# Performance work log

Hardware: AMD Instinct MI355X
Metric: run time of the kernel (lower is better)

The kernel has to match this reference:

```python
import jax, jax.numpy as jnp
import numpy as np

B, S, D = 4, 2048, 1024

def setup_inputs() -> dict:
    key = jax.random.key(0)
    k1, k2, k3, k4 = jax.random.split(key, 4)
    output = jax.random.normal(k1, (B, S, D), dtype=jnp.float32)
    # nn.Linear(dim, dim, bias=False): y = x @ W.T ; store W as [D, D]
    scale = 1.0 / np.sqrt(D)
    w_q = jax.random.uniform(k2, (D, D), dtype=jnp.float32, minval=-scale, maxval=scale)
    w_k = jax.random.uniform(k3, (D, D), dtype=jnp.float32, minval=-scale, maxval=scale)
    w_v = jax.random.uniform(k4, (D, D), dtype=jnp.float32, minval=-scale, maxval=scale)
    return {"output": output, "w_q": w_q, "w_k": w_k, "w_v": w_v}

def reference(output, w_q, w_k, w_v):
    # projections: x @ W.T (torch Linear convention)
    q = jnp.einsum('bsd,ed->bse', output, w_q)
    k = jnp.einsum('bsd,ed->bse', output, w_k)
    v = jnp.einsum('bsd,ed->bse', output, w_v)
    scores = jnp.einsum('bqd,bkd->bqk', q, k)      # unscaled, no mask
    attn = jax.nn.softmax(scores, axis=-1)
    return jnp.einsum('bqk,bkd->bqd', attn, v)
```

## Files before the change

### kernel.cpp

```cpp
#include <hip/hip_runtime.h>
#include <hip/hip_bf16.h>
#include <stdint.h>


typedef __attribute__((ext_vector_type(8))) _Float16 f16x8;
typedef __attribute__((ext_vector_type(4))) float f32x4;
typedef __attribute__((ext_vector_type(4))) unsigned short u16x4;

__device__ inline unsigned short f2h(float f) {
    union { _Float16 h; unsigned short u; } x;
    x.h = (_Float16)f;
    return x.u;
}
__device__ inline float h2f(unsigned short u) {
    union { unsigned short u; _Float16 h; } x;
    x.u = u;
    return (float)x.h;
}

__device__ inline void async16(const unsigned short* g, unsigned short* l) {
    __builtin_amdgcn_global_load_lds(
        (__attribute__((address_space(1))) void*)g,
        (__attribute__((address_space(3))) void*)l, 16, 0, 0);
}

template <int MODE, int BN>
__global__ __launch_bounds__(512)
void gemm512(const unsigned short* __restrict__ A,
             const unsigned short* __restrict__ B,
             void* __restrict__ C, void* __restrict__ C2,
             int K, int ldA, int ldB, int ldC,
             long sAz, long sBz, long sCz)
{
    constexpr int NT = BN / 32;
    constexpr int BI = BN / 64;
    __shared__ __align__(16) unsigned short smem[256 * 64 + BN * 64];
    unsigned short* As = smem;
    unsigned short* Bs = smem + 256 * 64;

    const int tid  = threadIdx.x;
    const int lane = tid & 63;
    const int wave = tid >> 6;
    const int wr   = wave >> 1, wc = wave & 1;
    const int quad = lane >> 4, lrow = lane & 15;
    const int bm   = blockIdx.x, bn = blockIdx.y, z = blockIdx.z;

    const unsigned short* Az = A + (long)z * sAz;
    const unsigned short* Bz = B + (long)z * sBz;

    const unsigned short* gA[4];
    const unsigned short* gB[BI];
#pragma unroll
    for (int i = 0; i < 4; ++i) {
        const int l = tid + 512 * i;
        const int r = l >> 3;
        const int c = (l & 7) ^ (r & 7);
        gA[i] = Az + (long)(bm * 256 + r) * ldA + c * 8;
    }
#pragma unroll
    for (int i = 0; i < BI; ++i) {
        const int l = tid + 512 * i;
        const int r = l >> 3;
        const int c = (l & 7) ^ (r & 7);
        gB[i] = Bz + (long)(bn * BN + r) * ldB + c * 8;
    }

    f32x4 acc[4][NT];
#pragma unroll
    for (int i = 0; i < 4; ++i)
#pragma unroll
        for (int j = 0; j < NT; ++j)
            acc[i][j] = f32x4{0.f, 0.f, 0.f, 0.f};

    const int fr = lrow & 7;

    for (int k0 = 0; k0 < K; k0 += 64) {
#pragma unroll
        for (int i = 0; i < 4; ++i) async16(gA[i], &As[(tid + 512 * i) * 8]);
#pragma unroll
        for (int i = 0; i < BI; ++i) async16(gB[i], &Bs[(tid + 512 * i) * 8]);
#pragma unroll
        for (int i = 0; i < 4; ++i) gA[i] += 64;
#pragma unroll
        for (int i = 0; i < BI; ++i) gB[i] += 64;
        __syncthreads();

#pragma unroll
        for (int ks = 0; ks < 2; ++ks) {
            const int pc = (((ks << 2) + quad) ^ fr) * 8;
            f16x8 af[4], bf[NT];
#pragma unroll
            for (int mt = 0; mt < 4; ++mt)
                af[mt] = *(const f16x8*)&As[(wr * 64 + mt * 16 + lrow) * 64 + pc];
#pragma unroll
            for (int nt = 0; nt < NT; ++nt)
                bf[nt] = *(const f16x8*)&Bs[(wc * (BN / 2) + nt * 16 + lrow) * 64 + pc];
#pragma unroll
            for (int mt = 0; mt < 4; ++mt)
#pragma unroll
                for (int nt = 0; nt < NT; ++nt)
                    acc[mt][nt] = __builtin_amdgcn_mfma_f32_16x16x32_f16(
                        af[mt], bf[nt], acc[mt][nt], 0, 0, 0);
        }
        __syncthreads();
    }

    const int col_base = bn * BN + wc * (BN / 2);

    if (MODE != 0 || z < 2) {
        const int row_base = bm * 256 + wr * 64;
        const long zC = (long)z * sCz;
#pragma unroll
        for (int mt = 0; mt < 4; ++mt)
#pragma unroll
            for (int nt = 0; nt < NT; ++nt)
#pragma unroll
                for (int r = 0; r < 4; ++r) {
                    const int row = row_base + mt * 16 + quad * 4 + r;
                    const int col = col_base + nt * 16 + lrow;
                    if (MODE == 2)
                        ((float*)C)[zC + (long)row * ldC + col] = acc[mt][nt][r];
                    else
                        ((unsigned short*)C)[zC + (long)row * ldC + col] =
                            f2h(acc[mt][nt][r]);
                }
    } else {
        unsigned short* T = smem;
#pragma unroll
        for (int p = 0; p < 4; ++p) {
            __syncthreads();
            if (wr == p) {
#pragma unroll
                for (int mt = 0; mt < 4; ++mt)
#pragma unroll
                    for (int nt = 0; nt < NT; ++nt) {
                        const int row_l = mt * 16 + quad * 4;
                        const int col_l = wc * 64 + nt * 16 + lrow;
                        u16x4 pk = {f2h(acc[mt][nt][0]), f2h(acc[mt][nt][1]),
                                    f2h(acc[mt][nt][2]), f2h(acc[mt][nt][3])};
                        *(u16x4*)&T[col_l * 72 + row_l] = pk;
                    }
            }
            __syncthreads();
            const int c  = tid >> 2;
            const int j0 = (tid & 3) * 16;
            const int tok0 = bm * 256 + p * 64;
            const int bb = tok0 >> 11;
            const int s0 = (tok0 & 2047) + j0;
            unsigned short* dst = (unsigned short*)C2 + (long)bb * 2097152 +
                                  (long)(bn * 128 + c) * 2048 + s0;
            const unsigned short* srcT = &T[c * 72 + j0];
            *(f16x8*)dst = *(const f16x8*)srcT;
            *(f16x8*)(dst + 8) = *(const f16x8*)(srcT + 8);
        }
    }
}

__global__ __launch_bounds__(256)
void cvt_all(const float* __restrict__ x, const float* __restrict__ w0,
             const float* __restrict__ w1, const float* __restrict__ w2,
             unsigned short* __restrict__ xh, unsigned short* __restrict__ wh)
{
    const int bid = blockIdx.x;
    const float* s;
    unsigned short* d;
    long i;
    if (bid < 4096) {
        s = x; d = xh;
        i = ((long)bid * 256 + threadIdx.x) * 8;
    } else {
        const int wid = bid - 4096;
        const int w = wid >> 9;
        s = (w == 0) ? w0 : (w == 1) ? w1 : w2;
        d = wh + (long)w * 1048576;
        i = ((long)(wid & 511) * 256 + threadIdx.x) * 8;
    }
    f32x4 a = *(const f32x4*)(s + i);
    f32x4 b = *(const f32x4*)(s + i + 4);
    union { unsigned short u[8]; f16x8 v; } t;
#pragma unroll
    for (int j = 0; j < 4; ++j) { t.u[j] = f2h(a[j]); t.u[4 + j] = f2h(b[j]); }
    *(f16x8*)(d + i) = t.v;
}

__global__ __launch_bounds__(256)
void softmax16(unsigned short* __restrict__ sc)
{
    const long row = blockIdx.x;
    unsigned short* srow = sc + row * 2048;
    const int tid = threadIdx.x;

    union { u16x4 p[2]; unsigned short u[8]; } in;
    in.p[0] = *(const u16x4*)(srow + tid * 8);
    in.p[1] = *(const u16x4*)(srow + tid * 8 + 4);
    float v[8];
#pragma unroll
    for (int i = 0; i < 8; ++i) v[i] = h2f(in.u[i]);

    float m = v[0];
#pragma unroll
    for (int i = 1; i < 8; ++i) m = fmaxf(m, v[i]);
#pragma unroll
    for (int off = 32; off; off >>= 1) m = fmaxf(m, __shfl_xor(m, off));

    __shared__ float redm[4], reds[4];
    if ((tid & 63) == 0) redm[tid >> 6] = m;
    __syncthreads();
    m = fmaxf(fmaxf(redm[0], redm[1]), fmaxf(redm[2], redm[3]));

    float s = 0.f;
#pragma unroll
    for (int i = 0; i < 8; ++i) { v[i] = __expf(v[i] - m); s += v[i]; }
#pragma unroll
    for (int off = 32; off; off >>= 1) s += __shfl_xor(s, off);
    if ((tid & 63) == 0) reds[tid >> 6] = s;
    __syncthreads();
    s = reds[0] + reds[1] + reds[2] + reds[3];

    const float inv = 1.f / s;
    union { unsigned short u[8]; f16x8 w; } t;
#pragma unroll
    for (int i = 0; i < 8; ++i) t.u[i] = f2h(v[i] * inv);
    *(f16x8*)(srow + tid * 8) = t.w;
}

extern "C" void kernel_launch(void* const* d_in, const int* in_sizes, int n_in,
                              void* d_out, int out_size, void* d_ws, size_t ws_size,
                              hipStream_t stream)
{
    const float* x  = (const float*)d_in[0];
    const float* wq = (const float*)d_in[1];
    const float* wk = (const float*)d_in[2];
    const float* wv = (const float*)d_in[3];
    float* out = (float*)d_out;

    char* base = (char*)d_ws;
    const bool batched = (ws_size >= 88080384UL);

    unsigned short* xh = (unsigned short*)base;
    unsigned short* wh = (unsigned short*)(base + 16777216);
    unsigned short* sc = (unsigned short*)base;
    unsigned short* q  = (unsigned short*)(base + (batched ? 33554432 : 23068672));
    unsigned short* k  = q + 8388608;
    unsigned short* vt = k + 8388608;

    cvt_all<<<5632, 256, 0, stream>>>(x, wq, wk, wv, xh, wh);

    gemm512<0, 128><<<dim3(32, 8, 3), 512, 0, stream>>>(
        xh, wh, q, vt, 1024, 1024, 1024, 1024, 0L, 1048576L, 8388608L);

    if (batched) {
        gemm512<1, 128><<<dim3(8, 16, 4), 512, 0, stream>>>(
            q, k, sc, nullptr, 1024, 1024, 1024, 2048,
            2097152L, 2097152L, 4194304L);
        softmax16<<<8192, 256, 0, stream>>>(sc);
        gemm512<2, 64><<<dim3(8, 16, 4), 512, 0, stream>>>(
            sc, vt, out, nullptr, 2048, 2048, 2048, 1024,
            4194304L, 2097152L, 2097152L);
    } else {
        for (int b = 0; b < 4; ++b) {
            gemm512<1, 128><<<dim3(8, 16, 1), 512, 0, stream>>>(
                q + (long)b * 2097152, k + (long)b * 2097152, sc, nullptr,
                1024, 1024, 1024, 2048, 0L, 0L, 0L);
            softmax16<<<2048, 256, 0, stream>>>(sc);
            gemm512<2, 64><<<dim3(8, 16, 1), 512, 0, stream>>>(
                sc, vt + (long)b * 2097152, out + (long)b * 2097152, nullptr,
                2048, 2048, 2048, 1024, 0L, 0L, 0L);
        }
    }
}
```

Before: 243.9 us.

## Switch GEMMs to 128x128 tiles with 2 waves using 32x32x16 MFMA

Replaces the 512-thread, 256-row-tile GEMM with a 128-thread kernel that computes 128x128 tiles, each wave owning a 128x64 slab. It uses the 32x32x16 f16 MFMA, which has higher operand reuse per instruction, and sets launch bounds for two blocks per CU. The epilogue and the transposed V store are rewritten for the 32x32 accumulator layout. Grids double, giving more blocks to fill the CUs, but each wave now needs many more accumulator registers and fewer waves are available to hide the unpipelined LDS load latency.

```diff
diff --git a/kernel.cpp b/kernel.cpp
--- a/kernel.cpp
+++ b/kernel.cpp
@@ -3,9 +3,10 @@
 #include <stdint.h>
 
 
-typedef __attribute__((ext_vector_type(8))) _Float16 f16x8;
-typedef __attribute__((ext_vector_type(4))) float f32x4;
-typedef __attribute__((ext_vector_type(4))) unsigned short u16x4;
+typedef __attribute__((ext_vector_type(8)))  _Float16 f16x8;
+typedef __attribute__((ext_vector_type(4)))  float    f32x4;
+typedef __attribute__((ext_vector_type(16))) float    f32x16;
+typedef __attribute__((ext_vector_type(4)))  unsigned short u16x4;
 
 __device__ inline unsigned short f2h(float f) {
     union { _Float16 h; unsigned short u; } x;
@@ -24,134 +25,133 @@
         (__attribute__((address_space(3))) void*)l, 16, 0, 0);
 }
 
-template <int MODE, int BN>
-__global__ __launch_bounds__(512)
-void gemm512(const unsigned short* __restrict__ A,
-             const unsigned short* __restrict__ B,
-             void* __restrict__ C, void* __restrict__ C2,
-             int K, int ldA, int ldB, int ldC,
-             long sAz, long sBz, long sCz)
-{
-    constexpr int NT = BN / 32;
-    constexpr int BI = BN / 64;
-    __shared__ __align__(16) unsigned short smem[256 * 64 + BN * 64];
+template <int MODE>
+__global__ __launch_bounds__(128, 2)
+void gemm32(const unsigned short* __restrict__ A,
+            const unsigned short* __restrict__ B,
+            void* __restrict__ C, void* __restrict__ C2,
+            int K, int ldA, int ldB, int ldC,
+            long sAz, long sBz, long sCz)
+{
+    __shared__ __align__(16) unsigned short smem[2 * 128 * 64];
     unsigned short* As = smem;
-    unsigned short* Bs = smem + 256 * 64;
+    unsigned short* Bs = smem + 128 * 64;
 
     const int tid  = threadIdx.x;
     const int lane = tid & 63;
-    const int wave = tid >> 6;
-    const int wr   = wave >> 1, wc = wave & 1;
-    const int quad = lane >> 4, lrow = lane & 15;
+    const int wc   = tid >> 6;
+    const int l31  = lane & 31;
+    const int h    = lane >> 5;
     const int bm   = blockIdx.x, bn = blockIdx.y, z = blockIdx.z;
 
     const unsigned short* Az = A + (long)z * sAz;
     const unsigned short* Bz = B + (long)z * sBz;
 
-    const unsigned short* gA[4];
-    const unsigned short* gB[BI];
-#pragma unroll
-    for (int i = 0; i < 4; ++i) {
-        const int l = tid + 512 * i;
+    const unsigned short* gA[8];
+    const unsigned short* gB[8];
+#pragma unroll
+    for (int i = 0; i < 8; ++i) {
+        const int l = tid + 128 * i;
         const int r = l >> 3;
         const int c = (l & 7) ^ (r & 7);
-        gA[i] = Az + (long)(bm * 256 + r) * ldA + c * 8;
-    }
-#pragma unroll
-    for (int i = 0; i < BI; ++i) {
-        const int l = tid + 512 * i;
-        const int r = l >> 3;
-        const int c = (l & 7) ^ (r & 7);
-        gB[i] = Bz + (long)(bn * BN + r) * ldB + c * 8;
-    }
-
-    f32x4 acc[4][NT];
+        gA[i] = Az + (long)(bm * 128 + r) * ldA + c * 8;
+        gB[i] = Bz + (long)(bn * 128 + r) * ldB + c * 8;
+    }
+
+    f32x16 acc[4][2];
 #pragma unroll
     for (int i = 0; i < 4; ++i)
 #pragma unroll
-        for (int j = 0; j < NT; ++j)
-            acc[i][j] = f32x4{0.f, 0.f, 0.f, 0.f};
-
-    const int fr = lrow & 7;
+        for (int j = 0; j < 2; ++j)
+            acc[i][j] = (f32x16)(0.f);
+
+    const int fr = lane & 7;
 
     for (int k0 = 0; k0 < K; k0 += 64) {
 #pragma unroll
-        for (int i = 0; i < 4; ++i) async16(gA[i], &As[(tid + 512 * i) * 8]);
-#pragma unroll
-        for (int i = 0; i < BI; ++i) async16(gB[i], &Bs[(tid + 512 * i) * 8]);
-#pragma unroll
-        for (int i = 0; i < 4; ++i) gA[i] += 64;
-#pragma unroll
-        for (int i = 0; i < BI; ++i) gB[i] += 64;
+        for (int i = 0; i < 8; ++i) async16(gA[i], &As[(tid + 128 * i) * 8]);
+#pragma unroll
+        for (int i = 0; i < 8; ++i) async16(gB[i], &Bs[(tid + 128 * i) * 8]);
+#pragma unroll
+        for (int i = 0; i < 8; ++i) { gA[i] += 64; gB[i] += 64; }
         __syncthreads();
 
 #pragma unroll
-        for (int ks = 0; ks < 2; ++ks) {
-            const int pc = (((ks << 2) + quad) ^ fr) * 8;
-            f16x8 af[4], bf[NT];
+        for (int s = 0; s < 4; ++s) {
+            const int pc = (((s << 1) + h) ^ fr) * 8;
+            f16x8 af[4], bf[2];
 #pragma unroll
             for (int mt = 0; mt < 4; ++mt)
-                af[mt] = *(const f16x8*)&As[(wr * 64 + mt * 16 + lrow) * 64 + pc];
-#pragma unroll
-            for (int nt = 0; nt < NT; ++nt)
-                bf[nt] = *(const f16x8*)&Bs[(wc * (BN / 2) + nt * 16 + lrow) * 64 + pc];
+                af[mt] = *(const f16x8*)&As[(mt * 32 + l31) * 64 + pc];
+#pragma unroll
+            for (int nt = 0; nt < 2; ++nt)
+                bf[nt] = *(const f16x8*)&Bs[(wc * 64 + nt * 32 + l31) * 64 + pc];
 #pragma unroll
             for (int mt = 0; mt < 4; ++mt)
 #pragma unroll
-                for (int nt = 0; nt < NT; ++nt)
-                    acc[mt][nt] = __builtin_amdgcn_mfma_f32_16x16x32_f16(
+                for (int nt = 0; nt < 2; ++nt)
+                    acc[mt][nt] = __builtin_amdgcn_mfma_f32_32x32x16_f16(
                         af[mt], bf[nt], acc[mt][nt], 0, 0, 0);
         }
         __syncthreads();
     }
 
-    const int col_base = bn * BN + wc * (BN / 2);
+    const int col_base = bn * 128 + wc * 64;
 
     if (MODE != 0 || z < 2) {
-        const int row_base = bm * 256 + wr * 64;
+        const int row_base = bm * 128;
         const long zC = (long)z * sCz;
 #pragma unroll
         for (int mt = 0; mt < 4; ++mt)
 #pragma unroll
-            for (int nt = 0; nt < NT; ++nt)
-#pragma unroll
-                for (int r = 0; r < 4; ++r) {
-                    const int row = row_base + mt * 16 + quad * 4 + r;
-                    const int col = col_base + nt * 16 + lrow;
-                    if (MODE == 2)
-                        ((float*)C)[zC + (long)row * ldC + col] = acc[mt][nt][r];
-                    else
-                        ((unsigned short*)C)[zC + (long)row * ldC + col] =
-                            f2h(acc[mt][nt][r]);
-                }
+            for (int nt = 0; nt < 2; ++nt)
+#pragma unroll
+                for (int g = 0; g < 4; ++g)
+#pragma unroll
+                    for (int r = 0; r < 4; ++r) {
+                        const int reg = g * 4 + r;
+                        const int row = row_base + mt * 32 + 4 * h + 8 * g + r;
+                        const int col = col_base + nt * 32 + l31;
+                        if (MODE == 2)
+                            ((float*)C)[zC + (long)row * ldC + col] =
+                                acc[mt][nt][reg];
+                        else
+                            ((unsigned short*)C)[zC + (long)row * ldC + col] =
+                                f2h(acc[mt][nt][reg]);
+                    }
     } else {
         unsigned short* T = smem;
 #pragma unroll
-        for (int p = 0; p < 4; ++p) {
+        for (int p = 0; p < 2; ++p) {
             __syncthreads();
-            if (wr == p) {
+            if (wc == p) {
 #pragma unroll
                 for (int mt = 0; mt < 4; ++mt)
 #pragma unroll
-                    for (int nt = 0; nt < NT; ++nt) {
-                        const int row_l = mt * 16 + quad * 4;
-                        const int col_l = wc * 64 + nt * 16 + lrow;
-                        u16x4 pk = {f2h(acc[mt][nt][0]), f2h(acc[mt][nt][1]),
-                                    f2h(acc[mt][nt][2]), f2h(acc[mt][nt][3])};
-                        *(u16x4*)&T[col_l * 72 + row_l] = pk;
-                    }
+                    for (int nt = 0; nt < 2; ++nt)
+#pragma unroll
+                        for (int g = 0; g < 4; ++g) {
+                            const int col_l = nt * 32 + l31;
+                            const int r0 = mt * 32 + 4 * h + 8 * g;
+                            u16x4 pk = {f2h(acc[mt][nt][g * 4 + 0]),
+                                        f2h(acc[mt][nt][g * 4 + 1]),
+                                        f2h(acc[mt][nt][g * 4 + 2]),
+                                        f2h(acc[mt][nt][g * 4 + 3])};
+                            *(u16x4*)&T[col_l * 136 + r0] = pk;
+                        }
             }
             __syncthreads();
-            const int c  = tid >> 2;
-            const int j0 = (tid & 3) * 16;
-            const int tok0 = bm * 256 + p * 64;
+            const int c  = tid >> 1;
+            const int j0 = (tid & 1) * 64;
+            const int tok0 = bm * 128;
             const int bb = tok0 >> 11;
             const int s0 = (tok0 & 2047) + j0;
             unsigned short* dst = (unsigned short*)C2 + (long)bb * 2097152 +
-                                  (long)(bn * 128 + c) * 2048 + s0;
-            const unsigned short* srcT = &T[c * 72 + j0];
-            *(f16x8*)dst = *(const f16x8*)srcT;
-            *(f16x8*)(dst + 8) = *(const f16x8*)(srcT + 8);
+                                  (long)(bn * 128 + p * 64 + c) * 2048 + s0;
+            const unsigned short* srcT = &T[c * 136 + j0];
+#pragma unroll
+            for (int i = 0; i < 8; ++i)
+                *(f16x8*)(dst + i * 8) = *(const f16x8*)(srcT + i * 8);
         }
     }
 }
@@ -246,24 +246,24 @@
 
     cvt_all<<<5632, 256, 0, stream>>>(x, wq, wk, wv, xh, wh);
 
-    gemm512<0, 128><<<dim3(32, 8, 3), 512, 0, stream>>>(
+    gemm32<0><<<dim3(64, 8, 3), 128, 0, stream>>>(
         xh, wh, q, vt, 1024, 1024, 1024, 1024, 0L, 1048576L, 8388608L);
 
     if (batched) {
-        gemm512<1, 128><<<dim3(8, 16, 4), 512, 0, stream>>>(
+        gemm32<1><<<dim3(16, 16, 4), 128, 0, stream>>>(
             q, k, sc, nullptr, 1024, 1024, 1024, 2048,
             2097152L, 2097152L, 4194304L);
         softmax16<<<8192, 256, 0, stream>>>(sc);
-        gemm512<2, 64><<<dim3(8, 16, 4), 512, 0, stream>>>(
+        gemm32<2><<<dim3(16, 8, 4), 128, 0, stream>>>(
             sc, vt, out, nullptr, 2048, 2048, 2048, 1024,
             4194304L, 2097152L, 2097152L);
     } else {
         for (int b = 0; b < 4; ++b) {
-            gemm512<1, 128><<<dim3(8, 16, 1), 512, 0, stream>>>(
+            gemm32<1><<<dim3(16, 16, 1), 128, 0, stream>>>(
                 q + (long)b * 2097152, k + (long)b * 2097152, sc, nullptr,
                 1024, 1024, 1024, 2048, 0L, 0L, 0L);
             softmax16<<<2048, 256, 0, stream>>>(sc);
-            gemm512<2, 64><<<dim3(8, 16, 1), 512, 0, stream>>>(
+            gemm32<2><<<dim3(16, 8, 1), 128, 0, stream>>>(
                 sc, vt + (long)b * 2097152, out + (long)b * 2097152, nullptr,
                 2048, 2048, 2048, 1024, 0L, 0L, 0L);
         }
```

Result: slower. 265.8 us (+9.0%).

## Double-buffer GEMM LDS tiles with K=32 stages to overlap loads and MFMA

Applied to the files above, without the earlier changes.

Replaces the single-buffered K=64 LDS tile with two K=32 buffers. The next tile's async global-to-LDS copy is issued before computing on the current one, so memory latency can overlap with MFMA work. The swizzle is adapted to 4-chunk rows, and BN<128 cases use a partial set of threads for B loads. Each K=32 step does less math per barrier, and the loop assumes K is a multiple of 64 because it steps by two stages.

```diff
diff --git a/kernel.cpp b/kernel.cpp
--- a/kernel.cpp
+++ b/kernel.cpp
@@ -32,11 +32,10 @@
              int K, int ldA, int ldB, int ldC,
              long sAz, long sBz, long sCz)
 {
-    constexpr int NT = BN / 32;
-    constexpr int BI = BN / 64;
-    __shared__ __align__(16) unsigned short smem[256 * 64 + BN * 64];
-    unsigned short* As = smem;
-    unsigned short* Bs = smem + 256 * 64;
+    constexpr int NT  = BN / 32;
+    constexpr int BCH = BN * 4;
+    constexpr int BUF = (256 + BN) * 32;
+    __shared__ __align__(16) unsigned short smem[2 * BUF];
 
     const int tid  = threadIdx.x;
     const int lane = tid & 63;
@@ -48,22 +47,13 @@
     const unsigned short* Az = A + (long)z * sAz;
     const unsigned short* Bz = B + (long)z * sBz;
 
-    const unsigned short* gA[4];
-    const unsigned short* gB[BI];
-#pragma unroll
-    for (int i = 0; i < 4; ++i) {
-        const int l = tid + 512 * i;
-        const int r = l >> 3;
-        const int c = (l & 7) ^ (r & 7);
-        gA[i] = Az + (long)(bm * 256 + r) * ldA + c * 8;
-    }
-#pragma unroll
-    for (int i = 0; i < BI; ++i) {
-        const int l = tid + 512 * i;
-        const int r = l >> 3;
-        const int c = (l & 7) ^ (r & 7);
-        gB[i] = Bz + (long)(bn * BN + r) * ldB + c * 8;
-    }
+    const int rA0 = tid >> 2,          cA0 = (tid & 3) ^ ((rA0 >> 1) & 3);
+    const int rA1 = (tid + 512) >> 2,  cA1 = (tid & 3) ^ ((rA1 >> 1) & 3);
+    const unsigned short* gA0 = Az + (long)(bm * 256 + rA0) * ldA + cA0 * 8;
+    const unsigned short* gA1 = Az + (long)(bm * 256 + rA1) * ldA + cA1 * 8;
+    const int rB0 = tid >> 2,          cB0 = (tid & 3) ^ ((rB0 >> 1) & 3);
+    const unsigned short* gB0 = (tid < BCH)
+        ? Bz + (long)(bn * BN + rB0) * ldB + cB0 * 8 : nullptr;
 
     f32x4 acc[4][NT];
 #pragma unroll
@@ -72,37 +62,48 @@
         for (int j = 0; j < NT; ++j)
             acc[i][j] = f32x4{0.f, 0.f, 0.f, 0.f};
 
-    const int fr = lrow & 7;
-
-    for (int k0 = 0; k0 < K; k0 += 64) {
-#pragma unroll
-        for (int i = 0; i < 4; ++i) async16(gA[i], &As[(tid + 512 * i) * 8]);
-#pragma unroll
-        for (int i = 0; i < BI; ++i) async16(gB[i], &Bs[(tid + 512 * i) * 8]);
-#pragma unroll
-        for (int i = 0; i < 4; ++i) gA[i] += 64;
-#pragma unroll
-        for (int i = 0; i < BI; ++i) gB[i] += 64;
+    const int pc = (quad ^ ((lrow >> 1) & 3)) * 8;
+
+    auto stage = [&](int b) {
+        unsigned short* As = smem + b * BUF;
+        unsigned short* Bs = As + 256 * 32;
+        async16(gA0, &As[tid * 8]);
+        async16(gA1, &As[(tid + 512) * 8]);
+        if (BCH == 512) {
+            async16(gB0, &Bs[tid * 8]);
+        } else if (tid < BCH) {
+            async16(gB0, &Bs[tid * 8]);
+        }
+        gA0 += 32; gA1 += 32;
+        if (BCH == 512 || tid < BCH) gB0 += 32;
+    };
+    auto compute = [&](int b) {
+        const unsigned short* As = smem + b * BUF;
+        const unsigned short* Bs = As + 256 * 32;
+        f16x8 af[4], bf[NT];
+#pragma unroll
+        for (int mt = 0; mt < 4; ++mt)
+            af[mt] = *(const f16x8*)&As[(wr * 64 + mt * 16 + lrow) * 32 + pc];
+#pragma unroll
+        for (int nt = 0; nt < NT; ++nt)
+            bf[nt] = *(const f16x8*)&Bs[(wc * (BN / 2) + nt * 16 + lrow) * 32 + pc];
+#pragma unroll
+        for (int mt = 0; mt < 4; ++mt)
+#pragma unroll
+            for (int nt = 0; nt < NT; ++nt)
+                acc[mt][nt] = __builtin_amdgcn_mfma_f32_16x16x32_f16(
+                    af[mt], bf[nt], acc[mt][nt], 0, 0, 0);
+    };
+
+    const int niter = K >> 5;
+    stage(0);
+    for (int i = 0; i < niter; i += 2) {
         __syncthreads();
-
-#pragma unroll
-        for (int ks = 0; ks < 2; ++ks) {
-            const int pc = (((ks << 2) + quad) ^ fr) * 8;
-            f16x8 af[4], bf[NT];
-#pragma unroll
-            for (int mt = 0; mt < 4; ++mt)
-                af[mt] = *(const f16x8*)&As[(wr * 64 + mt * 16 + lrow) * 64 + pc];
-#pragma unroll
-            for (int nt = 0; nt < NT; ++nt)
-                bf[nt] = *(const f16x8*)&Bs[(wc * (BN / 2) + nt * 16 + lrow) * 64 + pc];
-#pragma unroll
-            for (int mt = 0; mt < 4; ++mt)
-#pragma unroll
-                for (int nt = 0; nt < NT; ++nt)
-                    acc[mt][nt] = __builtin_amdgcn_mfma_f32_16x16x32_f16(
-                        af[mt], bf[nt], acc[mt][nt], 0, 0, 0);
-        }
+        if (i + 1 < niter) stage(1);
+        compute(0);
         __syncthreads();
+        if (i + 2 < niter) stage(0);
+        compute(1);
     }
 
     const int col_base = bn * BN + wc * (BN / 2);
```

New measurement: 293.4 us. +20.3%, slower.
